# Kernel tuning notes

Measured on AMD Instinct MI355X. Metric: run time of the kernel, lower is better.

Reference implementation:

```python
import jax, jax.numpy as jnp
import numpy as np

B, T, DIN, E, HA, HB = 16, 128, 1024, 128, 128, 128


def setup_inputs() -> dict:
    key = jax.random.key(0)
    ks = jax.random.split(key, 12)
    u = lambda k, shape: jax.random.uniform(k, shape, jnp.float32, -0.1, 0.1)
    return {
        "x": jax.random.normal(ks[0], (B, T, DIN), jnp.float32),
        "W_emb": u(ks[1], (E, DIN)),
        "Wih_a": u(ks[2], (3 * HA, E)),
        "Whh_a": u(ks[3], (3 * HA, HA)),
        "bih_a": jnp.zeros((3 * HA,), jnp.float32),
        "bhh_a": jnp.zeros((3 * HA,), jnp.float32),
        "Wa": u(ks[4], (1, HA)),
        "ba": jnp.zeros((1,), jnp.float32),
        "Wih_b": u(ks[5], (3 * HB, E)),
        "Whh_b": u(ks[6], (3 * HB, HB)),
        "bih_b": jnp.zeros((3 * HB,), jnp.float32),
        "bhh_b": jnp.zeros((3 * HB,), jnp.float32),
        "Wb": u(ks[7], (E, HB)),
        "bb": jnp.zeros((E,), jnp.float32),
        "Wo": u(ks[8], (1, E)),
        "bo": jnp.zeros((1,), jnp.float32),
    }


def _gru_scan(x_seq, Wih, Whh, bih, bhh):
    # x_seq: (L, Ti, B, D) -> hidden states (L, Ti, B, H), PyTorch GRU gate math.
    H = Whh.shape[1]

    def step(h, x):
        gi = jnp.einsum('tbd,gd->tbg', x, Wih) + bih
        gh = jnp.einsum('tbh,gh->tbg', h, Whh) + bhh
        i_r, i_z, i_n = jnp.split(gi, 3, axis=-1)
        h_r, h_z, h_n = jnp.split(gh, 3, axis=-1)
        r = jax.nn.sigmoid(i_r + h_r)
        z = jax.nn.sigmoid(i_z + h_z)
        n = jnp.tanh(i_n + r * h_n)
        h2 = (1.0 - z) * n + z * h
        return h2, h2

    h0 = jnp.zeros(x_seq.shape[1:-1] + (H,), x_seq.dtype)
    _, hs = jax.lax.scan(step, h0, x_seq)
    return hs


def reference(x, W_emb, Wih_a, Whh_a, bih_a, bhh_a, Wa, ba,
              Wih_b, Whh_b, bih_b, bhh_b, Wb, bb, Wo, bo):
    emb = jnp.einsum('btd,ed->bte', x, W_emb)  # (B,T,E)
    Tn = emb.shape[1]
    i_idx = jnp.arange(Tn)
    k_idx = jnp.arange(Tn)
    # idx[i,k] = i-k (clipped): position j = i-k of the reversed prefix ending at i.
    idx = jnp.clip(i_idx[:, None] - k_idx[None, :], 0)
    # X_rev[k,i,b,:] = emb[b, i-k]  (reversed prefix inputs for every i at once)
    X_rev = jnp.transpose(emb[:, idx], (2, 1, 0, 3))  # (Tk,Ti,B,E)
    # Step k of the scan consumes temb[i-k] for every i simultaneously; outputs at
    # k<=i depend only on valid inputs, so padding (clipped k>i) never pollutes them.
    hs_a = _gru_scan(X_rev, Wih_a, Whh_a, bih_a, bhh_a) * 0.5  # (Tk,Ti,B,HA)
    hs_b = _gru_scan(X_rev, Wih_b, Whh_b, bih_b, bhh_b) * 0.5  # (Tk,Ti,B,HB)
    pre_alpha = jnp.einsum('kibh,oh->kib', hs_a, Wa) + ba[0]   # (Tk,Ti,B)
    valid = (k_idx[:, None] <= i_idx[None, :])[:, :, None]     # (Tk,Ti,1)
    pre_alpha = jnp.where(valid, pre_alpha, -1e30)
    alpha = jax.nn.softmax(pre_alpha, axis=0)                  # softmax over prefix positions
    beta = jnp.tanh(jnp.einsum('kibh,eh->kibe', hs_b, Wb) + bb)
    # context c[b,i,:] = sum_j alpha*beta*emb[j]; emb_rev == X_rev since use_time=False.
    c = jnp.einsum('kib,kibe->bie', alpha, beta * X_rev)       # (B,T,E)
    logits = jnp.einsum('bie,oe->bi', c, Wo) + bo[0]           # (B,T)
    return logits
```

## Files before the change

kernel.cpp:

```cpp
#include <hip/hip_runtime.h>
#include <hip/hip_bf16.h>

typedef unsigned int uint;
typedef unsigned short ushort;
typedef __attribute__((ext_vector_type(8))) short bf16x8;
typedef __attribute__((ext_vector_type(4))) float f32x4;

#define Tn 128
#define Bn 16
#define HH 128
#define G3 384
#define DIN 1024
#define PAD 136
#define SQP 132

#if __has_builtin(__builtin_amdgcn_cvt_pk_bf16_f32)
__device__ __forceinline__ uint pack2(float a, float b){
    auto v = __builtin_amdgcn_cvt_pk_bf16_f32(a, b);
    union { decltype(v) v2; uint u; } c; c.v2 = v;
    return c.u;
}
#else
__device__ __forceinline__ ushort f2bf_(float f){
    union{float f; uint u;} c; c.f = f;
    uint u = c.u + 0x7fffu + ((c.u >> 16) & 1u);
    return (ushort)(u >> 16);
}
__device__ __forceinline__ uint pack2(float a, float b){
    return ((uint)f2bf_(b) << 16) | (uint)f2bf_(a);
}
#endif
__device__ __forceinline__ ushort f2bf(float f){ return (ushort)(pack2(f, f) & 0xffffu); }

#if __has_builtin(__builtin_amdgcn_fmed3f)
__device__ __forceinline__ float clampf(float x, float lo, float hi){
    return __builtin_amdgcn_fmed3f(x, lo, hi);
}
#else
__device__ __forceinline__ float clampf(float x, float lo, float hi){
    return fminf(hi, fmaxf(lo, x));
}
#endif

__device__ __forceinline__ float rcpf(float x){ return __builtin_amdgcn_rcpf(x); }
__device__ __forceinline__ float tanh_rat(float x){
    x = clampf(x, -5.f, 5.f);
    float t = x*x;
    float n = x*fmaf(t, fmaf(t, (t + 378.f), 17325.f), 135135.f);
    float d = fmaf(t, fmaf(t, fmaf(t, 28.f, 3150.f), 62370.f), 135135.f);
    return n * rcpf(d);
}
__device__ __forceinline__ float sig_num(float m, float t){
    return m*fmaf(t, fmaf(t, fmaf(t, 0.5f, 189.f), 8662.5f), 67567.5f);
}
__device__ __forceinline__ float sig_den(float t){
    return fmaf(t, fmaf(t, fmaf(t, 28.f, 3150.f), 62370.f), 135135.f);
}

__device__ __forceinline__ void bar_lds(){
    asm volatile("s_waitcnt lgkmcnt(0)\n\ts_barrier" ::: "memory");
}

__global__ __launch_bounds__(256) void k_cvt(const float* __restrict__ wemb,
                                             const float* __restrict__ wiha,
                                             const float* __restrict__ wihb,
                                             ushort* __restrict__ dst){
    int idx = (blockIdx.x*256 + threadIdx.x)*8;
    const float* s; int off;
    if (idx < 131072){ s = wemb; off = idx; }
    else if (idx < 180224){ s = wiha; off = idx - 131072; }
    else { s = wihb; off = idx - 180224; }
    float4 f0 = *(const float4*)(s + off);
    float4 f1 = *(const float4*)(s + off + 4);
    *(uint4*)(dst + idx) = (uint4){pack2(f0.x,f0.y),pack2(f0.z,f0.w),
                                   pack2(f1.x,f1.y),pack2(f1.z,f1.w)};
}

__device__ __forceinline__ const uint4* stage_src(int c, const ushort* WembB,
                                                  const ushort* WihaB,
                                                  const ushort* WihbB,
                                                  int wr2, int wc2){
    if (c < 8)  return (const uint4*)(WembB + (size_t)wr2*DIN + c*128 + wc2);
    if (c < 11) return (const uint4*)(WihaB + (size_t)((c-8)*128 + wr2)*HH + wc2);
    return (const uint4*)(WihbB + (size_t)((c-11)*128 + wr2)*HH + wc2);
}

__global__ __launch_bounds__(512) void k_embgi(
    const float* __restrict__ x,      const ushort* __restrict__ WembB,
    const ushort* __restrict__ WihaB, const ushort* __restrict__ WihbB,
    const float* __restrict__ biha,   const float* __restrict__ bhha,
    const float* __restrict__ bihb,   const float* __restrict__ bhhb,
    const float* __restrict__ Wo,
    float* __restrict__ gia, float* __restrict__ gib, float* __restrict__ woE)
{
    __shared__ __align__(16) ushort LX[2][16*PAD];
    __shared__ __align__(16) ushort LW[2][128*PAD];
    __shared__ __align__(16) ushort LE[16*PAD];
    int tid = threadIdx.x;
    int lane = tid & 63, wave = tid >> 6;
    int quad = lane >> 4, n = lane & 15;
    int R0 = blockIdx.x * 8;
    int xr = tid >> 6, xc = (tid & 63) * 2;
    int wr2 = tid >> 2, wc2 = (tid & 3) * 32;

    for (int z = tid; z < 544; z += 512){
        ((uint*)&LX[0][8*PAD])[z] = 0;
        ((uint*)&LX[1][8*PAD])[z] = 0;
        ((uint*)&LE[8*PAD])[z]    = 0;
    }
    {
        const uint4* s0 = stage_src(0, WembB, WihaB, WihbB, wr2, wc2);
        uint4 a0=s0[0], a1=s0[1], a2=s0[2], a3=s0[3];
        float2 v = *(const float2*)(x + (size_t)(R0 + xr)*DIN + xc);
        uint4* d = (uint4*)&LW[0][wr2*PAD + wc2];
        d[0]=a0; d[1]=a1; d[2]=a2; d[3]=a3;
        *(uint*)&LX[0][xr*PAD + xc] = pack2(v.x, v.y);
    }

    f32x4 acc = {0.f,0.f,0.f,0.f};
    for (int c = 0; c < 8; ++c){
        bar_lds();
        int cur = c & 1, nxt = cur ^ 1;
        const uint4* sn = stage_src(c+1, WembB, WihaB, WihbB, wr2, wc2);
        uint4 r0=sn[0], r1=sn[1], r2=sn[2], r3=sn[3];
        float2 vx = {0.f,0.f};
        if (c+1 < 8) vx = *(const float2*)(x + (size_t)(R0 + xr)*DIN + (c+1)*128 + xc);
#pragma unroll
        for (int kb = 0; kb < 4; ++kb){
            bf16x8 a = *(const bf16x8*)&LX[cur][n*PAD + kb*32 + quad*8];
            bf16x8 b = *(const bf16x8*)&LW[cur][(wave*16 + n)*PAD + kb*32 + quad*8];
            acc = __builtin_amdgcn_mfma_f32_16x16x32_bf16(a, b, acc, 0,0,0);
        }
        {
            uint4* d = (uint4*)&LW[nxt][wr2*PAD + wc2];
            d[0]=r0; d[1]=r1; d[2]=r2; d[3]=r3;
            if (c+1 < 8) *(uint*)&LX[nxt][xr*PAD + xc] = pack2(vx.x, vx.y);
        }
    }
    if (quad < 2){
        int e = wave*16 + n;
        float wo = Wo[e];
#pragma unroll
        for (int l = 0; l < 4; ++l){
            int m = quad*4 + l;
            LE[m*PAD + e] = f2bf(acc[l]);
            int row = R0 + m, b_ = row >> 7, pos = row & 127;
            woE[((size_t)(pos*Bn + b_))*HH + e] = wo * acc[l];
        }
    }
    for (int c = 8; c < 14; ++c){
        bar_lds();
        int cur = c & 1, nxt = cur ^ 1;
        uint4 r0, r1, r2, r3;
        if (c < 13){
            const uint4* sn = stage_src(c+1, WembB, WihaB, WihbB, wr2, wc2);
            r0=sn[0]; r1=sn[1]; r2=sn[2]; r3=sn[3];
        }
        f32x4 gc = {0.f,0.f,0.f,0.f};
#pragma unroll
        for (int kb = 0; kb < 4; ++kb){
            bf16x8 a = *(const bf16x8*)&LE[n*PAD + kb*32 + quad*8];
            bf16x8 b = *(const bf16x8*)&LW[cur][(wave*16 + n)*PAD + kb*32 + quad*8];
            gc = __builtin_amdgcn_mfma_f32_16x16x32_bf16(a, b, gc, 0,0,0);
        }
        int nc = c - 8;
        int gband = (nc < 3) ? nc : nc - 3;
        int g = gband*128 + wave*16 + n;
        const float* bi = (nc < 3) ? biha : bihb;
        const float* bh = (nc < 3) ? bhha : bhhb;
        float bias = bi[g] + ((gband < 2) ? bh[g] : 0.f);
        float scale = (gband < 2) ? 0.5f : 1.f;
        float* dst = (nc < 3) ? gia : gib;
        int P = (3*wave + gband)*16 + n;
        if (quad < 2){
#pragma unroll
            for (int l = 0; l < 4; ++l){
                int row = R0 + quad*4 + l, b_ = row >> 7, pos = row & 127;
                dst[((size_t)(pos*Bn + b_))*G3 + P] = scale*(gc[l] + bias);
            }
        }
        if (c < 13){
            uint4* d = (uint4*)&LW[nxt][wr2*PAD + wc2];
            d[0]=r0; d[1]=r1; d[2]=r2; d[3]=r3;
        }
    }
}

template<int GT>
__device__ __forceinline__ void gru_body(
    const float* __restrict__ Whh, const float* __restrict__ bhh,
    const float* __restrict__ Wsc, const float* __restrict__ bsc,
    const float* __restrict__ Gi,  const float* __restrict__ WoE,
    float* __restrict__ outW, int i)
{
    __shared__ __align__(16) ushort HF[2][2048];
    __shared__ __align__(16) ushort BFm[2][2048];
    __shared__ __align__(16) float SQ[16][SQP];
    int tid = threadIdx.x;
    int lane = tid & 63, wave = tid >> 6;
    int quad = lane >> 4, n = lane & 15;

    if (tid < 256) ((uint4*)HF[1])[tid] = (uint4){0,0,0,0};

    if (wave < 8){
        int u = wave, jb = u*16 + quad*4;
        bf16x8 afr[3][4];
#pragma unroll
        for (int g = 0; g < 3; ++g){
            const float* src = Whh + (size_t)(g*HH + u*16 + n)*HH;
            float s = (g < 2) ? 0.5f : 1.0f;
#pragma unroll
            for (int kb = 0; kb < 4; ++kb){
                const float* p = src + kb*32 + quad*8;
                float4 a = *(const float4*)p, b2 = *(const float4*)(p+4);
                union { uint4 q; bf16x8 v; } cv;
                cv.q.x = pack2(s*a.x, s*a.y);   cv.q.y = pack2(s*a.z, s*a.w);
                cv.q.z = pack2(s*b2.x,s*b2.y); cv.q.w = pack2(s*b2.z,s*b2.w);
                afr[g][kb] = cv.v;
            }
        }
        float bh2[4];
#pragma unroll
        for (int l = 0; l < 4; ++l) bh2[l] = bhh[2*HH + jb + l];
        float h4[4] = {0.f,0.f,0.f,0.f};

        const float* gp = Gi + ((size_t)(i*Bn + n))*G3 + u*48 + quad*4;
        float4 pg0 = *(const float4*)(gp);
        float4 pg1 = *(const float4*)(gp + 16);
        float4 pg2 = *(const float4*)(gp + 32);
        bar_lds();

        for (int k = 0; k <= i; ++k){
            int pos = i - k;
            float4 g0 = pg0, g1 = pg1, g2 = pg2;
            int pnext = (pos > 0) ? pos - 1 : 0;
            const float* gp2 = Gi + ((size_t)(pnext*Bn + n))*G3 + u*48 + quad*4;
            pg0 = *(const float4*)(gp2);
            pg1 = *(const float4*)(gp2 + 16);
            pg2 = *(const float4*)(gp2 + 32);

            const ushort* HR = HF[(k+1)&1];
            f32x4 a0={0.f,0.f,0.f,0.f}, a1=a0, a2=a0;
#pragma unroll
            for (int kb = 0; kb < 4; ++kb){
                bf16x8 bfr = *(const bf16x8*)&HR[(64*kb + lane)*8];
                a0 = __builtin_amdgcn_mfma_f32_16x16x32_bf16(afr[0][kb], bfr, a0, 0,0,0);
                a1 = __builtin_amdgcn_mfma_f32_16x16x32_bf16(afr[1][kb], bfr, a1, 0,0,0);
                a2 = __builtin_amdgcn_mfma_f32_16x16x32_bf16(afr[2][kb], bfr, a2, 0,0,0);
            }
            float gi0[4]={g0.x,g0.y,g0.z,g0.w};
            float gi1[4]={g1.x,g1.y,g1.z,g1.w};
            float gi2[4]={g2.x,g2.y,g2.z,g2.w};
#pragma unroll
            for (int l = 0; l < 4; ++l){
                float mr = clampf(gi0[l] + a0[l], -4.f, 4.f);
                float mz = clampf(gi1[l] + a1[l], -4.f, 4.f);
                float tr = mr*mr, tz = mz*mz;
                float nr = sig_num(mr, tr), nz = sig_num(mz, tz);
                float dr = sig_den(tr),     dz = sig_den(tz);
                float rD = rcpf(dr*dz);
                float r = fmaf(nr*dz, rD, 0.5f);
                float z = fmaf(nz*dr, rD, 0.5f);
                float nn = tanh_rat(gi2[l] + r*(a2[l] + bh2[l]));
                h4[l] = nn + z*(h4[l] - nn);
            }
            *(uint2*)&HF[k&1][((jb>>3)*16 + n)*8 + (jb&4)] =
                (uint2){pack2(h4[0],h4[1]), pack2(h4[2],h4[3])};
            bar_lds();
        }
        if (GT){ bar_lds(); bar_lds(); } else { bar_lds(); }
    } else {
        int u2 = wave - 8, jb = u2*16 + quad*4;
        if (GT){
            bf16x8 afr3[4];
#pragma unroll
            for (int kb = 0; kb < 4; ++kb){
                const float* p = Wsc + (size_t)(u2*16 + n)*HH + kb*32 + quad*8;
                float4 a = *(const float4*)p, b2 = *(const float4*)(p+4);
                union { uint4 q; bf16x8 v; } cv;
                cv.q.x = pack2(0.5f*a.x, 0.5f*a.y);  cv.q.y = pack2(0.5f*a.z, 0.5f*a.w);
                cv.q.z = pack2(0.5f*b2.x,0.5f*b2.y); cv.q.w = pack2(0.5f*b2.z,0.5f*b2.w);
                afr3[kb] = cv.v;
            }
            bf16x8 onesf;
            {
                union { uint4 q; bf16x8 v; } c1;
                uint o = (n == 0) ? 0x3F803F80u : 0u;
                c1.q = (uint4){o,o,o,o};
                onesf = c1.v;
            }
            float bb4[4];
#pragma unroll
            for (int l = 0; l < 4; ++l) bb4[l] = bsc[jb + l];
            float4 pwo = *(const float4*)(WoE + ((size_t)(i*Bn + n))*HH + jb);
            bar_lds();

            for (int k = 0; k <= i; ++k){
                int pos = i - k;
                float4 wo = pwo;
                pwo = *(const float4*)(WoE + ((size_t)(pos*Bn + n))*HH + jb);

                const ushort* HR = HF[(k+1)&1];
                f32x4 a3 = {0.f,0.f,0.f,0.f};
#pragma unroll
                for (int kb = 0; kb < 4; ++kb){
                    bf16x8 bfr = *(const bf16x8*)&HR[(64*kb + lane)*8];
                    a3 = __builtin_amdgcn_mfma_f32_16x16x32_bf16(afr3[kb], bfr, a3, 0,0,0);
                }
                if (u2 == 0 && k >= 2){
                    const ushort* BR = BFm[(k+1)&1];
                    f32x4 qa = {0.f,0.f,0.f,0.f};
#pragma unroll
                    for (int kb = 0; kb < 4; ++kb){
                        bf16x8 bq = *(const bf16x8*)&BR[(64*kb + lane)*8];
                        qa = __builtin_amdgcn_mfma_f32_16x16x32_bf16(onesf, bq, qa, 0,0,0);
                    }
                    if (lane < 16) SQ[lane][k-2] = qa[0];
                }
                if (k >= 1){
                    float w0 = tanh_rat(a3[0]+bb4[0])*wo.x;
                    float w1 = tanh_rat(a3[1]+bb4[1])*wo.y;
                    float w2 = tanh_rat(a3[2]+bb4[2])*wo.z;
                    float w3 = tanh_rat(a3[3]+bb4[3])*wo.w;
                    *(uint2*)&BFm[k&1][((jb>>3)*16 + n)*8 + (jb&4)] =
                        (uint2){pack2(w0,w1), pack2(w2,w3)};
                }
                bar_lds();
            }
            {
                const ushort* HR = HF[i&1];
                f32x4 a3 = {0.f,0.f,0.f,0.f};
#pragma unroll
                for (int kb = 0; kb < 4; ++kb){
                    bf16x8 bfr = *(const bf16x8*)&HR[(64*kb + lane)*8];
                    a3 = __builtin_amdgcn_mfma_f32_16x16x32_bf16(afr3[kb], bfr, a3, 0,0,0);
                }
                float w0 = tanh_rat(a3[0]+bb4[0])*pwo.x;
                float w1 = tanh_rat(a3[1]+bb4[1])*pwo.y;
                float w2 = tanh_rat(a3[2]+bb4[2])*pwo.z;
                float w3 = tanh_rat(a3[3]+bb4[3])*pwo.w;
                *(uint2*)&BFm[(i+1)&1][((jb>>3)*16 + n)*8 + (jb&4)] =
                    (uint2){pack2(w0,w1), pack2(w2,w3)};
            }
            bar_lds();
            if (u2 == 0){
                if (i >= 1){
                    const ushort* BR = BFm[i&1];
                    f32x4 qa = {0.f,0.f,0.f,0.f};
#pragma unroll
                    for (int kb = 0; kb < 4; ++kb){
                        bf16x8 bq = *(const bf16x8*)&BR[(64*kb + lane)*8];
                        qa = __builtin_amdgcn_mfma_f32_16x16x32_bf16(onesf, bq, qa, 0,0,0);
                    }
                    if (lane < 16) SQ[lane][i-1] = qa[0];
                }
                {
                    const ushort* BR = BFm[(i+1)&1];
                    f32x4 qa = {0.f,0.f,0.f,0.f};
#pragma unroll
                    for (int kb = 0; kb < 4; ++kb){
                        bf16x8 bq = *(const bf16x8*)&BR[(64*kb + lane)*8];
                        qa = __builtin_amdgcn_mfma_f32_16x16x32_bf16(onesf, bq, qa, 0,0,0);
                    }
                    if (lane < 16) SQ[lane][i] = qa[0];
                }
            }
            bar_lds();
        } else {
            if (u2 == 0){
                bf16x8 afr3[4];
#pragma unroll
                for (int kb = 0; kb < 4; ++kb){
                    const float* p = Wsc + kb*32 + quad*8;
                    float4 a = *(const float4*)p, b2 = *(const float4*)(p+4);
                    union { uint4 q; bf16x8 v; } cv;
                    if (n == 0){
                        cv.q.x = pack2(0.5f*a.x, 0.5f*a.y);  cv.q.y = pack2(0.5f*a.z, 0.5f*a.w);
                        cv.q.z = pack2(0.5f*b2.x,0.5f*b2.y); cv.q.w = pack2(0.5f*b2.z,0.5f*b2.w);
                    } else cv.q = (uint4){0,0,0,0};
                    afr3[kb] = cv.v;
                }
                float bav = bsc[0];
                bar_lds();
                for (int k = 0; k <= i; ++k){
                    if (k >= 1){
                        const ushort* HR = HF[(k+1)&1];
                        f32x4 a3 = {0.f,0.f,0.f,0.f};
#pragma unroll
                        for (int kb = 0; kb < 4; ++kb){
                            bf16x8 bfr = *(const bf16x8*)&HR[(64*kb + lane)*8];
                            a3 = __builtin_amdgcn_mfma_f32_16x16x32_bf16(afr3[kb], bfr, a3, 0,0,0);
                        }
                        if (lane < 16) SQ[lane][k-1] = a3[0] + bav;
                    }
                    bar_lds();
                }
                {
                    const ushort* HR = HF[i&1];
                    f32x4 a3 = {0.f,0.f,0.f,0.f};
#pragma unroll
                    for (int kb = 0; kb < 4; ++kb){
                        bf16x8 bfr = *(const bf16x8*)&HR[(64*kb + lane)*8];
                        a3 = __builtin_amdgcn_mfma_f32_16x16x32_bf16(afr3[kb], bfr, a3, 0,0,0);
                    }
                    if (lane < 16) SQ[lane][i] = a3[0] + bav;
                }
                bar_lds();
            } else {
                bar_lds();
                for (int k = 0; k <= i; ++k) bar_lds();
                bar_lds();
            }
        }
    }
    if (tid < 512){
        int cn = tid >> 5, k4 = (tid & 31) * 4;
        *(float4*)&outW[((size_t)(cn*Tn + i))*Tn + k4] = *(const float4*)&SQ[cn][k4];
    }
}

__global__ __launch_bounds__(1024, 1) void k_gru(
    const float* __restrict__ WhhA, const float* __restrict__ bhhA,
    const float* __restrict__ Wa,   const float* __restrict__ ba,
    const float* __restrict__ WhhB, const float* __restrict__ bhhB,
    const float* __restrict__ Wb,   const float* __restrict__ bb,
    const float* __restrict__ GiA,  const float* __restrict__ GiB,
    const float* __restrict__ WoE,
    float* __restrict__ sW, float* __restrict__ qW)
{
    int i = Tn - 1 - (blockIdx.x >> 1);
    if ((blockIdx.x & 1) == 0) gru_body<0>(WhhA, bhhA, Wa, ba, GiA, nullptr, sW, i);
    else                       gru_body<1>(WhhB, bhhB, Wb, bb, GiB, WoE,    qW, i);
}

__global__ __launch_bounds__(256) void k_out(const float* __restrict__ sW,
                                             const float* __restrict__ qW,
                                             const float* __restrict__ bo,
                                             float* __restrict__ out){
    int tid = threadIdx.x, lane = tid & 63, w = tid >> 6;
    int r = blockIdx.x*4 + w;
    int i = r & (Tn-1);
    const float* s = sW + (size_t)r*Tn;
    const float* q = qW + (size_t)r*Tn;
    float s0 = (lane     <= i) ? s[lane]      : -1e30f;
    float s1 = (64+lane  <= i) ? s[64+lane]   : -1e30f;
    float m = fmaxf(s0, s1);
#pragma unroll
    for (int off = 32; off; off >>= 1) m = fmaxf(m, __shfl_xor(m, off));
    float e0 = __expf(s0 - m), e1 = __expf(s1 - m);
    float q0 = (lane    <= i) ? q[lane]    : 0.f;
    float q1 = (64+lane <= i) ? q[64+lane] : 0.f;
    float num = e0*q0 + e1*q1, den = e0 + e1;
#pragma unroll
    for (int off = 32; off; off >>= 1){
        num += __shfl_xor(num, off);
        den += __shfl_xor(den, off);
    }
    if (lane == 0) out[r] = num/den + bo[0];
}

extern "C" void kernel_launch(void* const* d_in, const int* in_sizes, int n_in,
                              void* d_out, int out_size, void* d_ws, size_t ws_size,
                              hipStream_t stream) {
    const float* x     = (const float*)d_in[0];
    const float* Wemb  = (const float*)d_in[1];
    const float* Wih_a = (const float*)d_in[2];
    const float* Whh_a = (const float*)d_in[3];
    const float* bih_a = (const float*)d_in[4];
    const float* bhh_a = (const float*)d_in[5];
    const float* Wa    = (const float*)d_in[6];
    const float* ba    = (const float*)d_in[7];
    const float* Wih_b = (const float*)d_in[8];
    const float* Whh_b = (const float*)d_in[9];
    const float* bih_b = (const float*)d_in[10];
    const float* bhh_b = (const float*)d_in[11];
    const float* Wb    = (const float*)d_in[12];
    const float* bb    = (const float*)d_in[13];
    const float* Wo    = (const float*)d_in[14];
    const float* bo    = (const float*)d_in[15];

    const int NR = Bn*Tn;
    float* giA = (float*)d_ws;
    float* giB = giA + (size_t)NR*G3;
    float* woE = giB + (size_t)NR*G3;
    float* sW  = woE + (size_t)NR*HH;
    float* qW  = sW + (size_t)NR*Tn;
    ushort* wcv = (ushort*)(qW + (size_t)NR*Tn);
    ushort* wembB = wcv;
    ushort* wihaB = wcv + 131072;
    ushort* wihbB = wcv + 180224;

    k_cvt<<<dim3(112), 256, 0, stream>>>(Wemb, Wih_a, Wih_b, wcv);
    k_embgi<<<dim3(256), 512, 0, stream>>>(x, wembB, wihaB, wihbB,
                                           bih_a, bhh_a, bih_b, bhh_b, Wo,
                                           giA, giB, woE);
    k_gru<<<dim3(256), 1024, 0, stream>>>(Whh_a, bhh_a, Wa, ba,
                                          Whh_b, bhh_b, Wb, bb,
                                          giA, giB, woE, sW, qW);
    k_out<<<dim3(NR/4), 256, 0, stream>>>(sW, qW, bo, (float*)d_out);
}
```

Before: 248.1 us.

## Move score MFMA into recurrence waves and vectorize gate math with float2

The projection of hidden states by Wb (or Wa) moves from the auxiliary waves into the recurrent waves as a fourth MFMA accumulator. For the B branch its raw output goes through a double-buffered LDS buffer (ABF), and the auxiliary waves apply tanh and the Wo scaling one step later, which lengthens the pipeline by one stage. The gate nonlinearities are rewritten with float2 vectors so the compiler can emit packed FP32 ops. This aims to cut the per-step critical path and the duplicated LDS reads of hidden state, but it adds registers and extra barrier epilogue steps in the recurrent waves.

```diff
diff --git a/kernel.cpp b/kernel.cpp
--- a/kernel.cpp
+++ b/kernel.cpp
@@ -5,6 +5,7 @@
 typedef unsigned short ushort;
 typedef __attribute__((ext_vector_type(8))) short bf16x8;
 typedef __attribute__((ext_vector_type(4))) float f32x4;
+typedef __attribute__((ext_vector_type(2))) float f32x2;
 
 #define Tn 128
 #define Bn 16
@@ -13,6 +14,7 @@
 #define DIN 1024
 #define PAD 136
 #define SQP 132
+#define ABP 132
 
 #if __has_builtin(__builtin_amdgcn_cvt_pk_bf16_f32)
 __device__ __forceinline__ uint pack2(float a, float b){
@@ -43,18 +45,25 @@
 #endif
 
 __device__ __forceinline__ float rcpf(float x){ return __builtin_amdgcn_rcpf(x); }
+__device__ __forceinline__ f32x2 clamp2(f32x2 x, float lo, float hi){
+    f32x2 r; r.x = clampf(x.x, lo, hi); r.y = clampf(x.y, lo, hi); return r;
+}
+__device__ __forceinline__ f32x2 rcp2(f32x2 x){
+    f32x2 r; r.x = rcpf(x.x); r.y = rcpf(x.y); return r;
+}
+__device__ __forceinline__ f32x2 tanh2(f32x2 x){
+    x = clamp2(x, -5.f, 5.f);
+    f32x2 t = x*x;
+    f32x2 n = x*(t*(t*(t + 378.f) + 17325.f) + 135135.f);
+    f32x2 d = t*(t*(t*28.f + 3150.f) + 62370.f) + 135135.f;
+    return n * rcp2(d);
+}
 __device__ __forceinline__ float tanh_rat(float x){
     x = clampf(x, -5.f, 5.f);
     float t = x*x;
     float n = x*fmaf(t, fmaf(t, (t + 378.f), 17325.f), 135135.f);
     float d = fmaf(t, fmaf(t, fmaf(t, 28.f, 3150.f), 62370.f), 135135.f);
     return n * rcpf(d);
-}
-__device__ __forceinline__ float sig_num(float m, float t){
-    return m*fmaf(t, fmaf(t, fmaf(t, 0.5f, 189.f), 8662.5f), 67567.5f);
-}
-__device__ __forceinline__ float sig_den(float t){
-    return fmaf(t, fmaf(t, fmaf(t, 28.f, 3150.f), 62370.f), 135135.f);
 }
 
 __device__ __forceinline__ void bar_lds(){
@@ -195,6 +204,7 @@
 {
     __shared__ __align__(16) ushort HF[2][2048];
     __shared__ __align__(16) ushort BFm[2][2048];
+    __shared__ __align__(16) float ABF[2][16][ABP];
     __shared__ __align__(16) float SQ[16][SQP];
     int tid = threadIdx.x;
     int lane = tid & 63, wave = tid >> 6;
@@ -204,7 +214,7 @@
 
     if (wave < 8){
         int u = wave, jb = u*16 + quad*4;
-        bf16x8 afr[3][4];
+        bf16x8 afr[4][4];
 #pragma unroll
         for (int g = 0; g < 3; ++g){
             const float* src = Whh + (size_t)(g*HH + u*16 + n)*HH;
@@ -214,15 +224,33 @@
                 const float* p = src + kb*32 + quad*8;
                 float4 a = *(const float4*)p, b2 = *(const float4*)(p+4);
                 union { uint4 q; bf16x8 v; } cv;
-                cv.q.x = pack2(s*a.x, s*a.y);   cv.q.y = pack2(s*a.z, s*a.w);
+                cv.q.x = pack2(s*a.x, s*a.y);  cv.q.y = pack2(s*a.z, s*a.w);
                 cv.q.z = pack2(s*b2.x,s*b2.y); cv.q.w = pack2(s*b2.z,s*b2.w);
                 afr[g][kb] = cv.v;
             }
         }
-        float bh2[4];
-#pragma unroll
-        for (int l = 0; l < 4; ++l) bh2[l] = bhh[2*HH + jb + l];
-        float h4[4] = {0.f,0.f,0.f,0.f};
+#pragma unroll
+        for (int kb = 0; kb < 4; ++kb){
+            union { uint4 q; bf16x8 v; } cv;
+            cv.q = (uint4){0,0,0,0};
+            if (GT){
+                const float* p = Wsc + (size_t)(u*16 + n)*HH + kb*32 + quad*8;
+                float4 a = *(const float4*)p, b2 = *(const float4*)(p+4);
+                cv.q.x = pack2(0.5f*a.x, 0.5f*a.y);  cv.q.y = pack2(0.5f*a.z, 0.5f*a.w);
+                cv.q.z = pack2(0.5f*b2.x,0.5f*b2.y); cv.q.w = pack2(0.5f*b2.z,0.5f*b2.w);
+            } else if (u == 0 && n == 0){
+                const float* p = Wsc + kb*32 + quad*8;
+                float4 a = *(const float4*)p, b2 = *(const float4*)(p+4);
+                cv.q.x = pack2(0.5f*a.x, 0.5f*a.y);  cv.q.y = pack2(0.5f*a.z, 0.5f*a.w);
+                cv.q.z = pack2(0.5f*b2.x,0.5f*b2.y); cv.q.w = pack2(0.5f*b2.z,0.5f*b2.w);
+            }
+            afr[3][kb] = cv.v;
+        }
+        f32x2 bh2p[2];
+        bh2p[0] = (f32x2){bhh[2*HH + jb], bhh[2*HH + jb + 1]};
+        bh2p[1] = (f32x2){bhh[2*HH + jb + 2], bhh[2*HH + jb + 3]};
+        float bav = GT ? 0.f : bsc[0];
+        f32x2 h0 = {0.f,0.f}, h1 = {0.f,0.f};
 
         const float* gp = Gi + ((size_t)(i*Bn + n))*G3 + u*48 + quad*4;
         float4 pg0 = *(const float4*)(gp);
@@ -240,48 +268,66 @@
             pg2 = *(const float4*)(gp2 + 32);
 
             const ushort* HR = HF[(k+1)&1];
-            f32x4 a0={0.f,0.f,0.f,0.f}, a1=a0, a2=a0;
+            f32x4 a0={0.f,0.f,0.f,0.f}, a1=a0, a2=a0, a3=a0;
 #pragma unroll
             for (int kb = 0; kb < 4; ++kb){
                 bf16x8 bfr = *(const bf16x8*)&HR[(64*kb + lane)*8];
                 a0 = __builtin_amdgcn_mfma_f32_16x16x32_bf16(afr[0][kb], bfr, a0, 0,0,0);
                 a1 = __builtin_amdgcn_mfma_f32_16x16x32_bf16(afr[1][kb], bfr, a1, 0,0,0);
                 a2 = __builtin_amdgcn_mfma_f32_16x16x32_bf16(afr[2][kb], bfr, a2, 0,0,0);
-            }
-            float gi0[4]={g0.x,g0.y,g0.z,g0.w};
-            float gi1[4]={g1.x,g1.y,g1.z,g1.w};
-            float gi2[4]={g2.x,g2.y,g2.z,g2.w};
-#pragma unroll
-            for (int l = 0; l < 4; ++l){
-                float mr = clampf(gi0[l] + a0[l], -4.f, 4.f);
-                float mz = clampf(gi1[l] + a1[l], -4.f, 4.f);
-                float tr = mr*mr, tz = mz*mz;
-                float nr = sig_num(mr, tr), nz = sig_num(mz, tz);
-                float dr = sig_den(tr),     dz = sig_den(tz);
-                float rD = rcpf(dr*dz);
-                float r = fmaf(nr*dz, rD, 0.5f);
-                float z = fmaf(nz*dr, rD, 0.5f);
-                float nn = tanh_rat(gi2[l] + r*(a2[l] + bh2[l]));
-                h4[l] = nn + z*(h4[l] - nn);
+                if (GT || u == 0)
+                    a3 = __builtin_amdgcn_mfma_f32_16x16x32_bf16(afr[3][kb], bfr, a3, 0,0,0);
+            }
+            if (GT){
+                *(f32x4*)&ABF[(k+1)&1][n][jb] = a3;
+            } else if (u == 0 && k >= 1 && lane < 16){
+                SQ[lane][k-1] = a3[0] + bav;
+            }
+#pragma unroll
+            for (int p2 = 0; p2 < 2; ++p2){
+                f32x2 gi0 = p2 ? (f32x2){g0.z,g0.w} : (f32x2){g0.x,g0.y};
+                f32x2 gi1 = p2 ? (f32x2){g1.z,g1.w} : (f32x2){g1.x,g1.y};
+                f32x2 gi2 = p2 ? (f32x2){g2.z,g2.w} : (f32x2){g2.x,g2.y};
+                f32x2 a0p = p2 ? (f32x2){a0[2],a0[3]} : (f32x2){a0[0],a0[1]};
+                f32x2 a1p = p2 ? (f32x2){a1[2],a1[3]} : (f32x2){a1[0],a1[1]};
+                f32x2 a2p = p2 ? (f32x2){a2[2],a2[3]} : (f32x2){a2[0],a2[1]};
+                f32x2 mr = clamp2(gi0 + a0p, -4.f, 4.f);
+                f32x2 mz = clamp2(gi1 + a1p, -4.f, 4.f);
+                f32x2 tr = mr*mr, tz = mz*mz;
+                f32x2 nr = mr*(tr*(tr*(tr*0.5f + 189.f) + 8662.5f) + 67567.5f);
+                f32x2 nz = mz*(tz*(tz*(tz*0.5f + 189.f) + 8662.5f) + 67567.5f);
+                f32x2 dr = tr*(tr*(tr*28.f + 3150.f) + 62370.f) + 135135.f;
+                f32x2 dz = tz*(tz*(tz*28.f + 3150.f) + 62370.f) + 135135.f;
+                f32x2 rD = rcp2(dr*dz);
+                f32x2 r = nr*dz*rD + 0.5f;
+                f32x2 z = nz*dr*rD + 0.5f;
+                f32x2 nn = tanh2(gi2 + r*(a2p + bh2p[p2]));
+                if (p2 == 0) h0 = nn + z*(h0 - nn);
+                else         h1 = nn + z*(h1 - nn);
             }
             *(uint2*)&HF[k&1][((jb>>3)*16 + n)*8 + (jb&4)] =
-                (uint2){pack2(h4[0],h4[1]), pack2(h4[2],h4[3])};
+                (uint2){pack2(h0.x,h0.y), pack2(h1.x,h1.y)};
             bar_lds();
         }
-        if (GT){ bar_lds(); bar_lds(); } else { bar_lds(); }
+        {
+            const ushort* HR = HF[i&1];
+            if (GT || u == 0){
+                f32x4 a3 = {0.f,0.f,0.f,0.f};
+#pragma unroll
+                for (int kb = 0; kb < 4; ++kb){
+                    bf16x8 bfr = *(const bf16x8*)&HR[(64*kb + lane)*8];
+                    a3 = __builtin_amdgcn_mfma_f32_16x16x32_bf16(afr[3][kb], bfr, a3, 0,0,0);
+                }
+                if (GT) *(f32x4*)&ABF[i&1][n][jb] = a3;
+                else if (lane < 16) SQ[lane][i] = a3[0] + bav;
+            }
+            bar_lds();
+        }
+        bar_lds();
+        bar_lds();
     } else {
         int u2 = wave - 8, jb = u2*16 + quad*4;
         if (GT){
-            bf16x8 afr3[4];
-#pragma unroll
-            for (int kb = 0; kb < 4; ++kb){
-                const float* p = Wsc + (size_t)(u2*16 + n)*HH + kb*32 + quad*8;
-                float4 a = *(const float4*)p, b2 = *(const float4*)(p+4);
-                union { uint4 q; bf16x8 v; } cv;
-                cv.q.x = pack2(0.5f*a.x, 0.5f*a.y);  cv.q.y = pack2(0.5f*a.z, 0.5f*a.w);
-                cv.q.z = pack2(0.5f*b2.x,0.5f*b2.y); cv.q.w = pack2(0.5f*b2.z,0.5f*b2.w);
-                afr3[kb] = cv.v;
-            }
             bf16x8 onesf;
             {
                 union { uint4 q; bf16x8 v; } c1;
@@ -289,25 +335,14 @@
                 c1.q = (uint4){o,o,o,o};
                 onesf = c1.v;
             }
-            float bb4[4];
-#pragma unroll
-            for (int l = 0; l < 4; ++l) bb4[l] = bsc[jb + l];
-            float4 pwo = *(const float4*)(WoE + ((size_t)(i*Bn + n))*HH + jb);
+            f32x2 bb0 = {bsc[jb], bsc[jb+1]}, bb1 = {bsc[jb+2], bsc[jb+3]};
+            float4 woA = {0,0,0,0}, woB = {0,0,0,0}, woC = {0,0,0,0};
             bar_lds();
 
             for (int k = 0; k <= i; ++k){
-                int pos = i - k;
-                float4 wo = pwo;
-                pwo = *(const float4*)(WoE + ((size_t)(pos*Bn + n))*HH + jb);
-
-                const ushort* HR = HF[(k+1)&1];
-                f32x4 a3 = {0.f,0.f,0.f,0.f};
-#pragma unroll
-                for (int kb = 0; kb < 4; ++kb){
-                    bf16x8 bfr = *(const bf16x8*)&HR[(64*kb + lane)*8];
-                    a3 = __builtin_amdgcn_mfma_f32_16x16x32_bf16(afr3[kb], bfr, a3, 0,0,0);
-                }
-                if (u2 == 0 && k >= 2){
+                woA = woB; woB = woC;
+                woC = *(const float4*)(WoE + ((size_t)((i-k)*Bn + n))*HH + jb);
+                if (u2 == 0 && k >= 3){
                     const ushort* BR = BFm[(k+1)&1];
                     f32x4 qa = {0.f,0.f,0.f,0.f};
 #pragma unroll
@@ -315,37 +350,45 @@
                         bf16x8 bq = *(const bf16x8*)&BR[(64*kb + lane)*8];
                         qa = __builtin_amdgcn_mfma_f32_16x16x32_bf16(onesf, bq, qa, 0,0,0);
                     }
-                    if (lane < 16) SQ[lane][k-2] = qa[0];
-                }
-                if (k >= 1){
-                    float w0 = tanh_rat(a3[0]+bb4[0])*wo.x;
-                    float w1 = tanh_rat(a3[1]+bb4[1])*wo.y;
-                    float w2 = tanh_rat(a3[2]+bb4[2])*wo.z;
-                    float w3 = tanh_rat(a3[3]+bb4[3])*wo.w;
+                    if (lane < 16) SQ[lane][k-3] = qa[0];
+                }
+                if (k >= 2){
+                    f32x4 pb = *(const f32x4*)&ABF[k&1][n][jb];
+                    f32x2 w0 = tanh2((f32x2){pb[0],pb[1]} + bb0) * (f32x2){woA.x,woA.y};
+                    f32x2 w1 = tanh2((f32x2){pb[2],pb[3]} + bb1) * (f32x2){woA.z,woA.w};
                     *(uint2*)&BFm[k&1][((jb>>3)*16 + n)*8 + (jb&4)] =
-                        (uint2){pack2(w0,w1), pack2(w2,w3)};
+                        (uint2){pack2(w0.x,w0.y), pack2(w1.x,w1.y)};
                 }
                 bar_lds();
             }
             {
-                const ushort* HR = HF[i&1];
-                f32x4 a3 = {0.f,0.f,0.f,0.f};
-#pragma unroll
-                for (int kb = 0; kb < 4; ++kb){
-                    bf16x8 bfr = *(const bf16x8*)&HR[(64*kb + lane)*8];
-                    a3 = __builtin_amdgcn_mfma_f32_16x16x32_bf16(afr3[kb], bfr, a3, 0,0,0);
-                }
-                float w0 = tanh_rat(a3[0]+bb4[0])*pwo.x;
-                float w1 = tanh_rat(a3[1]+bb4[1])*pwo.y;
-                float w2 = tanh_rat(a3[2]+bb4[2])*pwo.z;
-                float w3 = tanh_rat(a3[3]+bb4[3])*pwo.w;
-                *(uint2*)&BFm[(i+1)&1][((jb>>3)*16 + n)*8 + (jb&4)] =
-                    (uint2){pack2(w0,w1), pack2(w2,w3)};
-            }
-            bar_lds();
-            if (u2 == 0){
                 if (i >= 1){
+                    f32x4 pb = *(const f32x4*)&ABF[(i+1)&1][n][jb];
+                    f32x2 w0 = tanh2((f32x2){pb[0],pb[1]} + bb0) * (f32x2){woB.x,woB.y};
+                    f32x2 w1 = tanh2((f32x2){pb[2],pb[3]} + bb1) * (f32x2){woB.z,woB.w};
+                    *(uint2*)&BFm[(i+1)&1][((jb>>3)*16 + n)*8 + (jb&4)] =
+                        (uint2){pack2(w0.x,w0.y), pack2(w1.x,w1.y)};
+                }
+                if (u2 == 0 && i >= 2){
                     const ushort* BR = BFm[i&1];
+                    f32x4 qa = {0.f,0.f,0.f,0.f};
+#pragma unroll
+                    for (int kb = 0; kb < 4; ++kb){
+                        bf16x8 bq = *(const bf16x8*)&BR[(64*kb + lane)*8];
+                        qa = __builtin_amdgcn_mfma_f32_16x16x32_bf16(onesf, bq, qa, 0,0,0);
+                    }
+                    if (lane < 16) SQ[lane][i-2] = qa[0];
+                }
+                bar_lds();
+            }
+            {
+                f32x4 pb = *(const f32x4*)&ABF[i&1][n][jb];
+                f32x2 w0 = tanh2((f32x2){pb[0],pb[1]} + bb0) * (f32x2){woC.x,woC.y};
+                f32x2 w1 = tanh2((f32x2){pb[2],pb[3]} + bb1) * (f32x2){woC.z,woC.w};
+                *(uint2*)&BFm[i&1][((jb>>3)*16 + n)*8 + (jb&4)] =
+                    (uint2){pack2(w0.x,w0.y), pack2(w1.x,w1.y)};
+                if (u2 == 0 && i >= 1){
+                    const ushort* BR = BFm[(i+1)&1];
                     f32x4 qa = {0.f,0.f,0.f,0.f};
 #pragma unroll
                     for (int kb = 0; kb < 4; ++kb){
@@ -354,8 +397,11 @@
                     }
                     if (lane < 16) SQ[lane][i-1] = qa[0];
                 }
-                {
-                    const ushort* BR = BFm[(i+1)&1];
+                bar_lds();
+            }
+            {
+                if (u2 == 0){
+                    const ushort* BR = BFm[i&1];
                     f32x4 qa = {0.f,0.f,0.f,0.f};
 #pragma unroll
                     for (int kb = 0; kb < 4; ++kb){
@@ -364,53 +410,12 @@
                     }
                     if (lane < 16) SQ[lane][i] = qa[0];
                 }
-            }
+                bar_lds();
+            }
+        } else {
             bar_lds();
-        } else {
-            if (u2 == 0){
-                bf16x8 afr3[4];
-#pragma unroll
-                for (int kb = 0; kb < 4; ++kb){
-                    const float* p = Wsc + kb*32 + quad*8;
-                    float4 a = *(const float4*)p, b2 = *(const float4*)(p+4);
-                    union { uint4 q; bf16x8 v; } cv;
-                    if (n == 0){
-                        cv.q.x = pack2(0.5f*a.x, 0.5f*a.y);  cv.q.y = pack2(0.5f*a.z, 0.5f*a.w);
-                        cv.q.z = pack2(0.5f*b2.x,0.5f*b2.y); cv.q.w = pack2(0.5f*b2.z,0.5f*b2.w);
-                    } else cv.q = (uint4){0,0,0,0};
-                    afr3[kb] = cv.v;
-                }
-                float bav = bsc[0];
-                bar_lds();
-                for (int k = 0; k <= i; ++k){
-                    if (k >= 1){
-                        const ushort* HR = HF[(k+1)&1];
-                        f32x4 a3 = {0.f,0.f,0.f,0.f};
-#pragma unroll
-                        for (int kb = 0; kb < 4; ++kb){
-                            bf16x8 bfr = *(const bf16x8*)&HR[(64*kb + lane)*8];
-                            a3 = __builtin_amdgcn_mfma_f32_16x16x32_bf16(afr3[kb], bfr, a3, 0,0,0);
-                        }
-                        if (lane < 16) SQ[lane][k-1] = a3[0] + bav;
-                    }
-                    bar_lds();
-                }
-                {
-                    const ushort* HR = HF[i&1];
-                    f32x4 a3 = {0.f,0.f,0.f,0.f};
-#pragma unroll
-                    for (int kb = 0; kb < 4; ++kb){
-                        bf16x8 bfr = *(const bf16x8*)&HR[(64*kb + lane)*8];
-                        a3 = __builtin_amdgcn_mfma_f32_16x16x32_bf16(afr3[kb], bfr, a3, 0,0,0);
-                    }
-                    if (lane < 16) SQ[lane][i] = a3[0] + bav;
-                }
-                bar_lds();
-            } else {
-                bar_lds();
-                for (int k = 0; k <= i; ++k) bar_lds();
-                bar_lds();
-            }
+            for (int k = 0; k <= i; ++k) bar_lds();
+            bar_lds(); bar_lds(); bar_lds();
         }
     }
     if (tid < 512){
```

Result: slower. 275.1 us (+10.9%).
